# Optimization experiments

Measured on AMD Instinct MI355X. Metric: run time of the kernel, lower is better.

## Reference

```python
import jax, jax.numpy as jnp
import numpy as np

B, S, D, H = 4, 512, 1024, 16
HD = D // H
K_TOP = 8
MC_K = 8
EPS6 = 1e-6


def _affine(loc, scale, W, b):
    # Gaussian-diag affine: mu = x@W.T+b, var = scale^2 @ (W^2).T
    mu = loc @ W.T + b
    var = (scale ** 2) @ (W ** 2).T
    return mu, jnp.sqrt(var)


def _split(x):  # [B,S,D] -> [B,H,S,HD]
    return x.reshape(B, S, H, HD).transpose(0, 2, 1, 3)


def _combine(x):  # [B,H,S,HD] -> [B,S,D]
    return x.transpose(0, 2, 1, 3).reshape(B, S, D)


def _softmax_logit_normal(mu, var, excl_mask):
    # logit-normal softmax moment approximation (probit / delta method),
    # excluding masked positions (prob -> 0 there).
    adj = mu / jnp.sqrt(1.0 + (jnp.pi / 8.0) * var)
    adj = jnp.where(excl_mask, -1e9, adj)
    p = jax.nn.softmax(adj, axis=-1)
    v = (p * (1.0 - p)) ** 2 * var
    return p, v


def _forward(Q_loc, Q_scale, K_loc, K_scale, V_loc, V_scale,
             Wq, bq, Wk, bk, Wv, bv, Wo, bo, tau, eps):
    q_mu, q_sc = _affine(Q_loc, Q_scale, Wq, bq)
    k_mu, k_sc = _affine(K_loc, K_scale, Wk, bk)
    v_mu, v_sc = _affine(V_loc, V_scale, Wv, bv)

    # split heads; GaussianDiag round-trip adds 1e-6 to scale before squaring
    qm, qv = _split(q_mu), (_split(q_sc) + EPS6) ** 2
    km, kv = _split(k_mu), (_split(k_sc) + EPS6) ** 2
    vm, vv = _split(v_mu), (_split(v_sc) + EPS6) ** 2

    # bilinear moment: E[QK^T], Var[QK^T]
    S_mu = jnp.einsum('bhqd,bhkd->bhqk', qm, km)
    S_var = (jnp.einsum('bhqd,bhkd->bhqk', qm ** 2, kv)
             + jnp.einsum('bhqd,bhkd->bhqk', qv, km ** 2)
             + jnp.einsum('bhqd,bhkd->bhqk', qv, kv)) + EPS6

    s_mu = S_mu / jnp.sqrt(jnp.float32(HD))
    s_var = S_var / HD + EPS6

    l_mu = s_mu / tau
    l_var = s_var / (tau ** 2) + EPS6

    # top-k indices by mean logit
    topk_idx = jax.lax.top_k(l_mu, K_TOP)[1]  # [B,H,S,K_TOP]
    rows = jnp.arange(B * H * S)[:, None]
    mask = jnp.zeros((B * H * S, S), bool).at[rows, topk_idx.reshape(-1, K_TOP)].set(True)
    mask = mask.reshape(B, H, S, S)

    # MC-sample softmax (mc_k=8)
    std = jnp.sqrt(jnp.maximum(l_var, 1e-9))
    p_mean = jax.nn.softmax(l_mu[None] + std[None] * eps, axis=-1).mean(axis=0)

    # rest (non-top-k) logit-normal softmax moments
    rest_mean, rest_var = _softmax_logit_normal(l_mu, l_var, mask)

    top_out = jnp.where(mask, p_mean, rest_mean)
    top_out = top_out / jnp.maximum(top_out.sum(axis=-1, keepdims=True), 1e-12)

    # combine_top_rest: means add (variances do not feed the output path)
    attn_mu = top_out + rest_mean

    # linear combination with V distribution
    Y_mu = jnp.einsum('bhqk,bhkd->bhqd', attn_mu, vm)
    Y_var = jnp.einsum('bhqk,bhkd->bhqd', attn_mu ** 2, vv)
    Y_scale = jnp.sqrt(Y_var + EPS6)

    y_loc = _combine(Y_mu)
    y_scale = _combine(Y_scale) + EPS6

    out_loc = y_loc @ Wo.T + bo
    out_scale = jnp.sqrt((y_scale ** 2) @ (Wo ** 2).T)
    return out_loc, out_scale


def setup_inputs() -> dict:
    key = jax.random.key(0)
    ks = jax.random.split(key, 17)
    f32 = jnp.float32
    inp = {
        'Q_loc': jax.random.normal(ks[0], (B, S, D), f32),
        'Q_scale': jax.random.uniform(ks[1], (B, S, D), f32),
        'K_loc': jax.random.normal(ks[2], (B, S, D), f32),
        'K_scale': jax.random.uniform(ks[3], (B, S, D), f32),
        'V_loc': jax.random.normal(ks[4], (B, S, D), f32),
        'V_scale': jax.random.uniform(ks[5], (B, S, D), f32),
        'Wq': jax.random.normal(ks[6], (D, D), f32) * 0.02,
        'bq': jnp.zeros((D,), f32),
        'Wk': jax.random.normal(ks[7], (D, D), f32) * 0.02,
        'bk': jnp.zeros((D,), f32),
        'Wv': jax.random.normal(ks[8], (D, D), f32) * 0.02,
        'bv': jnp.zeros((D,), f32),
        'Wo': jax.random.normal(ks[9], (D, D), f32) * 0.02,
        'bo': jnp.zeros((D,), f32),
        'tau': jnp.array(1.0, f32),
        'eps': jax.random.normal(ks[10], (MC_K, B, H, S, S), f32),
    }
    return inp


def reference(Q_loc, Q_scale, K_loc, K_scale, V_loc, V_scale,
              Wq, bq, Wk, bk, Wv, bv, Wo, bo, tau, eps):
    return _forward(Q_loc, Q_scale, K_loc, K_scale, V_loc, V_scale,
                    Wq, bq, Wk, bk, Wv, bv, Wo, bo, tau, eps)
```

## Files before the change

kernel.cpp:

```cpp
#include <hip/hip_runtime.h>
#include <math.h>

#define B_ 4
#define S_ 512
#define D_ 1024
#define H_ 16
#define MCK 8
#define MS 2048
#define BHSS_ ((size_t)16777216)
#define BHS_  ((size_t)32768)

typedef __attribute__((ext_vector_type(8))) __bf16 bf16x8;
typedef __attribute__((ext_vector_type(4))) __bf16 bf16x4;
typedef __attribute__((ext_vector_type(4))) float f32x4;

__device__ __forceinline__ f32x4 mfma16(bf16x8 a, bf16x8 b, f32x4 c) {
  return __builtin_amdgcn_mfma_f32_16x16x32_bf16(a, b, c, 0, 0, 0);
}
__device__ __forceinline__ bf16x8 sq8(bf16x8 x) {
  bf16x8 r;
#pragma unroll
  for (int i = 0; i < 8; ++i) { float f = (float)x[i]; r[i] = (__bf16)(f * f); }
  return r;
}
__device__ __forceinline__ bf16x8 sq8s(bf16x8 h, bf16x8 l) {
  bf16x8 r;
#pragma unroll
  for (int i = 0; i < 8; ++i) { float f = (float)h[i] + (float)l[i]; r[i] = (__bf16)(f * f); }
  return r;
}
__device__ __forceinline__ float wave_max(float v) {
#pragma unroll
  for (int o = 32; o; o >>= 1) v = fmaxf(v, __shfl_xor(v, o));
  return v;
}
__device__ __forceinline__ float wave_sum(float v) {
#pragma unroll
  for (int o = 32; o; o >>= 1) v += __shfl_xor(v, o);
  return v;
}

__device__ __forceinline__ void unswz(int u, int& row, int& slot) {
  int row0 = ((u >> 2) ^ (u >> 4)) & 1;
  row = ((u >> 3) << 1) | row0;
  int s0 = (u ^ (u >> 2) ^ (u >> 4)) & 1;
  int s1 = ((u >> 1) ^ (u >> 3)) & 1;
  slot = (s1 << 1) | s0;
}
__device__ __forceinline__ int swz_el(int row, int slot) {
  return ((row * 4 + slot) ^ (row & 7)) * 8;
}
__device__ __forceinline__ void glds16(const void* gsrc, void* ldst) {
  __builtin_amdgcn_global_load_lds(
      (const __attribute__((address_space(1))) void*)gsrc,
      (__attribute__((address_space(3))) void*)ldst, 16, 0, 0);
}

__global__ __launch_bounds__(256) void conv_all(
    const float* __restrict__ l0, const float* __restrict__ s0,
    const float* __restrict__ l1, const float* __restrict__ s1,
    const float* __restrict__ l2, const float* __restrict__ s2,
    __bf16* h0, __bf16* o0, __bf16* v0,
    __bf16* h1, __bf16* o1, __bf16* v1,
    __bf16* h2, __bf16* o2, __bf16* v2,
    const float* __restrict__ w0, const float* __restrict__ w1,
    const float* __restrict__ w2, const float* __restrict__ w3,
    __bf16* wh0, __bf16* wo0, __bf16* wh1, __bf16* wo1,
    __bf16* wh2, __bf16* wo2, __bf16* wh3, __bf16* wo3)
{
  const int bid = blockIdx.x;
  if (bid < 3072) {
    const int tn = bid >> 10;
    const size_t i0 = ((size_t)(bid & 1023) * 256 + threadIdx.x) * 8;
    const float* L = tn == 0 ? l0 : tn == 1 ? l1 : l2;
    const float* S = tn == 0 ? s0 : tn == 1 ? s1 : s2;
    __bf16* Hh = tn == 0 ? h0 : tn == 1 ? h1 : h2;
    __bf16* Lo = tn == 0 ? o0 : tn == 1 ? o1 : o2;
    __bf16* V2 = tn == 0 ? v0 : tn == 1 ? v1 : v2;
    float4 x0 = *(const float4*)(L + i0), x1 = *(const float4*)(L + i0 + 4);
    float4 y0 = *(const float4*)(S + i0), y1 = *(const float4*)(S + i0 + 4);
    float xs[8] = {x0.x, x0.y, x0.z, x0.w, x1.x, x1.y, x1.z, x1.w};
    float ys[8] = {y0.x, y0.y, y0.z, y0.w, y1.x, y1.y, y1.z, y1.w};
    bf16x8 hh, ll, vv;
#pragma unroll
    for (int i = 0; i < 8; ++i) {
      __bf16 h = (__bf16)xs[i];
      hh[i] = h;
      ll[i] = (__bf16)(xs[i] - (float)h);
      vv[i] = (__bf16)(ys[i] * ys[i]);
    }
    *(bf16x8*)(Hh + i0) = hh;
    *(bf16x8*)(Lo + i0) = ll;
    *(bf16x8*)(V2 + i0) = vv;
  } else {
    const int b2 = bid - 3072;
    const int tn = b2 >> 9;
    const size_t i0 = ((size_t)(b2 & 511) * 256 + threadIdx.x) * 8;
    const float* W = tn == 0 ? w0 : tn == 1 ? w1 : tn == 2 ? w2 : w3;
    __bf16* Hh = tn == 0 ? wh0 : tn == 1 ? wh1 : tn == 2 ? wh2 : wh3;
    __bf16* Lo = tn == 0 ? wo0 : tn == 1 ? wo1 : tn == 2 ? wo2 : wo3;
    float4 x0 = *(const float4*)(W + i0), x1 = *(const float4*)(W + i0 + 4);
    float xs[8] = {x0.x, x0.y, x0.z, x0.w, x1.x, x1.y, x1.z, x1.w};
    bf16x8 hh, ll;
#pragma unroll
    for (int i = 0; i < 8; ++i) {
      __bf16 h = (__bf16)xs[i];
      hh[i] = h;
      ll[i] = (__bf16)(xs[i] - (float)h);
    }
    *(bf16x8*)(Hh + i0) = hh;
    *(bf16x8*)(Lo + i0) = ll;
  }
}

struct PArg {
  const __bf16 *Ah, *Al, *A2, *Wh, *Wl;
  const float* bias;
  __bf16 *P0, *P1, *P2, *P3;
  int epi;
};
struct PArg3 { PArg a[3]; };

#define LDSBUF 14336

__global__ __launch_bounds__(256, 2) void dgemm_qkv(PArg3 P3v)
{
  __shared__ __bf16 lds[2 * LDSBUF];
  const int lin = blockIdx.x + 8 * blockIdx.y + 256 * blockIdx.z;
  const int xcd = lin & 7;
  const int rest = lin >> 3;
  const int mi   = rest & 3;
  const int nblk = (rest >> 2) & 7;
  const int proj = rest >> 5;
  const PArg p = P3v.a[proj];
  const int m0 = (xcd + 8 * mi) * 64;
  const int n0 = nblk * 128;
  const int t = threadIdx.x, lane = t & 63, wid = t >> 6;
  int rA, sA; unswz(t, rA, sA);
  const size_t gA = (size_t)(m0 + rA) * D_ + sA * 8;
  const size_t gW0 = (size_t)(n0 + rA) * D_ + sA * 8;
  int rW1, sW1; unswz(t + 256, rW1, sW1);
  const size_t gW1 = (size_t)(n0 + rW1) * D_ + sW1 * 8;
  const int wofs = wid * 512;
  f32x4 accM[4][2] = {}; f32x4 accV[4][2] = {};
  const int fr = lane & 15, ks = lane >> 4;

  auto STAGE = [&](int buf, int k0) {
    __bf16* L = lds + buf * LDSBUF;
    glds16(p.Ah + gA + k0,  L + 0     + wofs);
    glds16(p.Al + gA + k0,  L + 2048  + wofs);
    glds16(p.A2 + gA + k0,  L + 4096  + wofs);
    glds16(p.Wh + gW0 + k0, L + 6144  + wofs);
    glds16(p.Wl + gW0 + k0, L + 10240 + wofs);
    glds16(p.Wh + gW1 + k0, L + 6144 + 2048 + wofs);
    glds16(p.Wl + gW1 + k0, L + 10240 + 2048 + wofs);
  };

  STAGE(0, 0);
  for (int tt = 0; tt < 32; ++tt) {
    const int cur = tt & 1;
    if (tt < 31) {
      STAGE(cur ^ 1, (tt + 1) * 32);
      asm volatile("s_waitcnt vmcnt(7)" ::: "memory");
    } else {
      asm volatile("s_waitcnt vmcnt(0)" ::: "memory");
    }
    __builtin_amdgcn_s_barrier();
    __builtin_amdgcn_sched_barrier(0);
    const __bf16* L = lds + cur * LDSBUF;
    bf16x8 fah[4], fal[4], fa2[4];
#pragma unroll
    for (int i = 0; i < 4; ++i) {
      int so = swz_el(i * 16 + fr, ks);
      fah[i] = *(const bf16x8*)(L + 0 + so);
      fal[i] = *(const bf16x8*)(L + 2048 + so);
      fa2[i] = *(const bf16x8*)(L + 4096 + so);
    }
#pragma unroll
    for (int j = 0; j < 2; ++j) {
      int so = swz_el(wid * 32 + j * 16 + fr, ks);
      bf16x8 fwh = *(const bf16x8*)(L + 6144 + so);
      bf16x8 fwl = *(const bf16x8*)(L + 10240 + so);
      bf16x8 fw2 = sq8s(fwh, fwl);
#pragma unroll
      for (int i = 0; i < 4; ++i) {
        accM[i][j] = mfma16(fah[i], fwh, accM[i][j]);
        accM[i][j] = mfma16(fah[i], fwl, accM[i][j]);
        accM[i][j] = mfma16(fal[i], fwh, accM[i][j]);
        accV[i][j] = mfma16(fa2[i], fw2, accV[i][j]);
      }
    }
    __builtin_amdgcn_s_barrier();
  }
  const int fq = lane >> 4;
#pragma unroll
  for (int j = 0; j < 2; ++j) {
    const int col = n0 + wid * 32 + j * 16 + fr;
    const float bcol = p.bias[col];
#pragma unroll
    for (int i = 0; i < 4; ++i) {
      const int row0 = m0 + i * 16 + fq * 4;
      f32x4 m_ = accM[i][j], v_ = accV[i][j];
      if (p.epi == 0) {
#pragma unroll
        for (int r = 0; r < 4; ++r) {
          size_t off = (size_t)(row0 + r) * D_ + col;
          float mu = m_[r] + bcol;
          __bf16 h = (__bf16)mu;
          float s = sqrtf(v_[r]) + 1e-6f;
          p.P0[off] = h;
          p.P1[off] = (__bf16)(mu - (float)h);
          p.P2[off] = (__bf16)(mu * mu);
          p.P3[off] = (__bf16)(s * s);
        }
      } else {
        const int b = row0 >> 9, ss0 = row0 & 511;
        const int hh = col >> 6, dd = col & 63;
        size_t base = ((size_t)(b * H_ + hh) * 64 + dd) * S_ + ss0;
        bf16x4 vh, vl, vq;
#pragma unroll
        for (int r = 0; r < 4; ++r) {
          float mu = m_[r] + bcol;
          __bf16 h = (__bf16)mu;
          vh[r] = h;
          vl[r] = (__bf16)(mu - (float)h);
          float s = sqrtf(v_[r]) + 1e-6f;
          vq[r] = (__bf16)(s * s);
        }
        *(bf16x4*)(p.P0 + base) = vh;
        *(bf16x4*)(p.P1 + base) = vl;
        *(bf16x4*)(p.P2 + base) = vq;
      }
    }
  }
}

__global__ __launch_bounds__(256, 2) void dgemm_o(
    const __bf16* __restrict__ Ah, const __bf16* __restrict__ Al, const __bf16* __restrict__ A2,
    const __bf16* __restrict__ Wh, const __bf16* __restrict__ Wl,
    const float* __restrict__ bias, float* __restrict__ O0, float* __restrict__ O1)
{
  __shared__ __bf16 lds[2 * LDSBUF];
  const int lin = blockIdx.x + 8 * blockIdx.y;
  const int xcd = lin & 7;
  const int rest = lin >> 3;
  const int mi   = rest & 3;
  const int nblk = rest >> 2;
  const int m0 = (xcd + 8 * mi) * 64;
  const int n0 = nblk * 128;
  const int t = threadIdx.x, lane = t & 63, wid = t >> 6;
  int rA, sA; unswz(t, rA, sA);
  const size_t gA = (size_t)(m0 + rA) * D_ + sA * 8;
  const size_t gW0 = (size_t)(n0 + rA) * D_ + sA * 8;
  int rW1, sW1; unswz(t + 256, rW1, sW1);
  const size_t gW1 = (size_t)(n0 + rW1) * D_ + sW1 * 8;
  const int wofs = wid * 512;
  f32x4 accM[4][2] = {}; f32x4 accV[4][2] = {};
  const int fr = lane & 15, ks = lane >> 4;

  auto STAGE = [&](int buf, int k0) {
    __bf16* L = lds + buf * LDSBUF;
    glds16(Ah + gA + k0,  L + 0     + wofs);
    glds16(Al + gA + k0,  L + 2048  + wofs);
    glds16(A2 + gA + k0,  L + 4096  + wofs);
    glds16(Wh + gW0 + k0, L + 6144  + wofs);
    glds16(Wl + gW0 + k0, L + 10240 + wofs);
    glds16(Wh + gW1 + k0, L + 6144 + 2048 + wofs);
    glds16(Wl + gW1 + k0, L + 10240 + 2048 + wofs);
  };

  STAGE(0, 0);
  for (int tt = 0; tt < 32; ++tt) {
    const int cur = tt & 1;
    if (tt < 31) {
      STAGE(cur ^ 1, (tt + 1) * 32);
      asm volatile("s_waitcnt vmcnt(7)" ::: "memory");
    } else {
      asm volatile("s_waitcnt vmcnt(0)" ::: "memory");
    }
    __builtin_amdgcn_s_barrier();
    __builtin_amdgcn_sched_barrier(0);
    const __bf16* L = lds + cur * LDSBUF;
    bf16x8 fah[4], fal[4], fa2[4];
#pragma unroll
    for (int i = 0; i < 4; ++i) {
      int so = swz_el(i * 16 + fr, ks);
      fah[i] = *(const bf16x8*)(L + 0 + so);
      fal[i] = *(const bf16x8*)(L + 2048 + so);
      fa2[i] = *(const bf16x8*)(L + 4096 + so);
    }
#pragma unroll
    for (int j = 0; j < 2; ++j) {
      int so = swz_el(wid * 32 + j * 16 + fr, ks);
      bf16x8 fwh = *(const bf16x8*)(L + 6144 + so);
      bf16x8 fwl = *(const bf16x8*)(L + 10240 + so);
      bf16x8 fw2 = sq8s(fwh, fwl);
#pragma unroll
      for (int i = 0; i < 4; ++i) {
        accM[i][j] = mfma16(fah[i], fwh, accM[i][j]);
        accM[i][j] = mfma16(fah[i], fwl, accM[i][j]);
        accM[i][j] = mfma16(fal[i], fwh, accM[i][j]);
        accV[i][j] = mfma16(fa2[i], fw2, accV[i][j]);
      }
    }
    __builtin_amdgcn_s_barrier();
  }
  const int fq = lane >> 4;
#pragma unroll
  for (int j = 0; j < 2; ++j) {
    const int col = n0 + wid * 32 + j * 16 + fr;
    const float bcol = bias[col];
#pragma unroll
    for (int i = 0; i < 4; ++i) {
      const int row0 = m0 + i * 16 + fq * 4;
      f32x4 m_ = accM[i][j], v_ = accV[i][j];
#pragma unroll
      for (int r = 0; r < 4; ++r) {
        size_t off = (size_t)(row0 + r) * D_ + col;
        O0[off] = m_[r] + bcol;
        O1[off] = sqrtf(v_[r]);
      }
    }
  }
}

__global__ __launch_bounds__(256) void score_mfma(
    const __bf16* __restrict__ qh, const __bf16* __restrict__ ql,
    const __bf16* __restrict__ q2, const __bf16* __restrict__ qv,
    const __bf16* __restrict__ kh, const __bf16* __restrict__ kl,
    const __bf16* __restrict__ k2, const __bf16* __restrict__ kv,
    float* __restrict__ lmu, __bf16* __restrict__ lvar,
    const float* __restrict__ taup)
{
  __shared__ __bf16 sQ[4][64][32];
  __shared__ __bf16 sK[4][64][32];
  const int t = threadIdx.x;
  const int lane = t & 63, wid = t >> 6;
  const int wm = wid >> 1, wn = wid & 1;
  const int lin = blockIdx.x + 8 * blockIdx.y + 64 * blockIdx.z;
  const int xcd = lin & 7;
  const int rest = lin >> 3;
  const int tile = rest & 63;
  const int bh = xcd + 8 * (rest >> 6);
  const int kk0 = (tile & 7) * 64, q0 = (tile >> 3) * 64;
  const int b = bh >> 4, h = bh & 15;
  const size_t hb = ((size_t)b * S_) * D_ + (size_t)h * 64;
  f32x4 accM[2][2] = {}; f32x4 accV[2][2] = {};
  const int crow = t >> 2, ccol = (t & 3) * 8;
  for (int d0 = 0; d0 < 64; d0 += 32) {
    size_t gq = hb + (size_t)(q0 + crow) * D_ + d0 + ccol;
    size_t gk = hb + (size_t)(kk0 + crow) * D_ + d0 + ccol;
    bf16x8 a0 = *(const bf16x8*)(qh + gq);
    bf16x8 a1 = *(const bf16x8*)(ql + gq);
    bf16x8 a2 = *(const bf16x8*)(q2 + gq);
    bf16x8 a3 = *(const bf16x8*)(qv + gq);
    bf16x8 b0 = *(const bf16x8*)(kh + gk);
    bf16x8 b1 = *(const bf16x8*)(kl + gk);
    bf16x8 b2 = *(const bf16x8*)(k2 + gk);
    bf16x8 b3 = *(const bf16x8*)(kv + gk);
    __syncthreads();
    *(bf16x8*)&sQ[0][crow][ccol] = a0;
    *(bf16x8*)&sQ[1][crow][ccol] = a1;
    *(bf16x8*)&sQ[2][crow][ccol] = a2;
    *(bf16x8*)&sQ[3][crow][ccol] = a3;
    *(bf16x8*)&sK[0][crow][ccol] = b0;
    *(bf16x8*)&sK[1][crow][ccol] = b1;
    *(bf16x8*)&sK[2][crow][ccol] = b2;
    *(bf16x8*)&sK[3][crow][ccol] = b3;
    __syncthreads();
    const int fr = lane & 15, kc = (lane >> 4) * 8;
    bf16x8 fqh[2], fql[2], fq2[2], fqv[2];
#pragma unroll
    for (int i = 0; i < 2; ++i) {
      int r = wm * 32 + i * 16 + fr;
      fqh[i] = *(const bf16x8*)&sQ[0][r][kc];
      fql[i] = *(const bf16x8*)&sQ[1][r][kc];
      fq2[i] = *(const bf16x8*)&sQ[2][r][kc];
      fqv[i] = *(const bf16x8*)&sQ[3][r][kc];
    }
#pragma unroll
    for (int j = 0; j < 2; ++j) {
      int r = wn * 32 + j * 16 + fr;
      bf16x8 fkh = *(const bf16x8*)&sK[0][r][kc];
      bf16x8 fkl = *(const bf16x8*)&sK[1][r][kc];
      bf16x8 fk2 = *(const bf16x8*)&sK[2][r][kc];
      bf16x8 fkv = *(const bf16x8*)&sK[3][r][kc];
#pragma unroll
      for (int i = 0; i < 2; ++i) {
        accM[i][j] = mfma16(fqh[i], fkh, accM[i][j]);
        accM[i][j] = mfma16(fqh[i], fkl, accM[i][j]);
        accM[i][j] = mfma16(fql[i], fkh, accM[i][j]);
        accV[i][j] = mfma16(fq2[i], fkv, accV[i][j]);
        accV[i][j] = mfma16(fqv[i], fk2, accV[i][j]);
        accV[i][j] = mfma16(fqv[i], fkv, accV[i][j]);
      }
    }
  }
  const float itau = 1.0f / *taup;
  const int fr = lane & 15, fq = lane >> 4;
#pragma unroll
  for (int i = 0; i < 2; ++i)
#pragma unroll
    for (int j = 0; j < 2; ++j) {
      const int col = kk0 + wn * 32 + j * 16 + fr;
      const int row0 = q0 + wm * 32 + i * 16 + fq * 4;
      f32x4 m_ = accM[i][j], v_ = accV[i][j];
#pragma unroll
      for (int r = 0; r < 4; ++r) {
        size_t off = ((size_t)bh * S_ + row0 + r) * S_ + col;
        lmu[off] = m_[r] * 0.125f * itau;
        float lv = ((v_[r] + 1e-6f) * (1.0f / 64.0f) + 1e-6f) * itau * itau + 1e-6f;
        lvar[off] = (__bf16)lv;
      }
    }
}

__global__ __launch_bounds__(256) void attn_kernel(
    const float* __restrict__ lmu, const __bf16* __restrict__ lvar,
    const float* __restrict__ eps, __bf16* __restrict__ ah, __bf16* __restrict__ al)
{
  const int wid = threadIdx.x >> 6;
  const int lane = threadIdx.x & 63;
  const size_t r = (size_t)blockIdx.x * 4 + wid;
  const float* mrow = lmu + r * S_;
  const __bf16* vrow = lvar + r * S_;
  const int c0 = lane * 4;
  float mu[8], va[8], sd[8];
  {
    float4 m0 = *(const float4*)(mrow + c0);
    float4 m1 = *(const float4*)(mrow + 256 + c0);
    mu[0] = m0.x; mu[1] = m0.y; mu[2] = m0.z; mu[3] = m0.w;
    mu[4] = m1.x; mu[5] = m1.y; mu[6] = m1.z; mu[7] = m1.w;
    bf16x4 v0 = *(const bf16x4*)(vrow + c0);
    bf16x4 v1 = *(const bf16x4*)(vrow + 256 + c0);
#pragma unroll
    for (int i = 0; i < 4; ++i) { va[i] = (float)v0[i]; va[4 + i] = (float)v1[i]; }
  }
#pragma unroll
  for (int i = 0; i < 8; ++i) sd[i] = sqrtf(fmaxf(va[i], 1e-9f));
  unsigned sel = 0;
  float x[8];
#pragma unroll
  for (int i = 0; i < 8; ++i) x[i] = mu[i];
  for (int tsel = 0; tsel < 8; ++tsel) {
    float bv = -INFINITY; int bi = 0x7fffffff;
#pragma unroll
    for (int i = 0; i < 8; ++i) {
      int gi = (i < 4) ? (c0 + i) : (256 + c0 + i - 4);
      if (x[i] > bv || (x[i] == bv && gi < bi)) { bv = x[i]; bi = gi; }
    }
    for (int o = 32; o; o >>= 1) {
      float ov = __shfl_xor(bv, o); int oi = __shfl_xor(bi, o);
      if (ov > bv || (ov == bv && oi < bi)) { bv = ov; bi = oi; }
    }
    int half = bi >> 8;
    int rem = bi & 255;
    if ((rem >> 2) == lane) {
      int slot = (rem & 3) + 4 * half;
      sel |= 1u << slot;
      x[slot] = -INFINITY;
    }
  }
  float pacc[8] = {0, 0, 0, 0, 0, 0, 0, 0};
  for (int mc = 0; mc < MCK; ++mc) {
    const float* ep = eps + (size_t)mc * BHSS_ + r * S_;
    float4 e0 = *(const float4*)(ep + c0);
    float4 e1 = *(const float4*)(ep + 256 + c0);
    float xv[8];
    xv[0] = mu[0] + sd[0] * e0.x; xv[1] = mu[1] + sd[1] * e0.y;
    xv[2] = mu[2] + sd[2] * e0.z; xv[3] = mu[3] + sd[3] * e0.w;
    xv[4] = mu[4] + sd[4] * e1.x; xv[5] = mu[5] + sd[5] * e1.y;
    xv[6] = mu[6] + sd[6] * e1.z; xv[7] = mu[7] + sd[7] * e1.w;
    float m = -INFINITY;
#pragma unroll
    for (int i = 0; i < 8; ++i) m = fmaxf(m, xv[i]);
    m = wave_max(m);
    float e[8], zs = 0.f;
#pragma unroll
    for (int i = 0; i < 8; ++i) { e[i] = __expf(xv[i] - m); zs += e[i]; }
    zs = wave_sum(zs);
    float inv = 1.0f / zs;
#pragma unroll
    for (int i = 0; i < 8; ++i) pacc[i] += e[i] * inv;
  }
  float adj[8];
#pragma unroll
  for (int i = 0; i < 8; ++i) {
    float a = mu[i] / sqrtf(1.0f + 0.39269908169872414f * va[i]);
    adj[i] = ((sel >> i) & 1u) ? -1e9f : a;
  }
  float m2 = -INFINITY;
#pragma unroll
  for (int i = 0; i < 8; ++i) m2 = fmaxf(m2, adj[i]);
  m2 = wave_max(m2);
  float e2[8], z2 = 0.f;
#pragma unroll
  for (int i = 0; i < 8; ++i) { e2[i] = __expf(adj[i] - m2); z2 += e2[i]; }
  z2 = wave_sum(z2);
  float inv2 = 1.0f / z2;
  float rest[8], tout[8], s = 0.f;
#pragma unroll
  for (int i = 0; i < 8; ++i) {
    rest[i] = e2[i] * inv2;
    tout[i] = ((sel >> i) & 1u) ? pacc[i] * 0.125f : rest[i];
    s += tout[i];
  }
  s = wave_sum(s);
  float rn = 1.0f / fmaxf(s, 1e-12f);
  bf16x4 oh0, oh1, ol0, ol1;
#pragma unroll
  for (int i = 0; i < 4; ++i) {
    float o = tout[i] * rn + rest[i];
    __bf16 h = (__bf16)o;
    oh0[i] = h; ol0[i] = (__bf16)(o - (float)h);
    float o1 = tout[4 + i] * rn + rest[4 + i];
    __bf16 h1 = (__bf16)o1;
    oh1[i] = h1; ol1[i] = (__bf16)(o1 - (float)h1);
  }
  *(bf16x4*)(ah + r * S_ + c0) = oh0;
  *(bf16x4*)(ah + r * S_ + 256 + c0) = oh1;
  *(bf16x4*)(al + r * S_ + c0) = ol0;
  *(bf16x4*)(al + r * S_ + 256 + c0) = ol1;
}

__global__ __launch_bounds__(256) void pv_mfma(
    const __bf16* __restrict__ ah_, const __bf16* __restrict__ al_,
    const __bf16* __restrict__ vTh, const __bf16* __restrict__ vTl,
    const __bf16* __restrict__ vTv,
    __bf16* __restrict__ yh, __bf16* __restrict__ yl, __bf16* __restrict__ ys2)
{
  __shared__ __bf16 sA[2][64][32];
  __shared__ __bf16 sV[3][64][32];
  const int t = threadIdx.x;
  const int lane = t & 63, wid = t >> 6;
  const int wm = wid >> 1, wn = wid & 1;
  const int lin = blockIdx.x + 8 * blockIdx.y;
  const int xcd = lin & 7;
  const int rest = lin >> 3;
  const int q0 = (rest & 7) * 64;
  const int bh = xcd + 8 * (rest >> 3);
  const int b = bh >> 4, h = bh & 15;
  const __bf16* Ah = ah_ + (size_t)bh * S_ * S_;
  const __bf16* Al = al_ + (size_t)bh * S_ * S_;
  const __bf16* Vh = vTh + (size_t)bh * 64 * S_;
  const __bf16* Vl = vTl + (size_t)bh * 64 * S_;
  const __bf16* Vv = vTv + (size_t)bh * 64 * S_;
  f32x4 accM[2][2] = {}; f32x4 accV[2][2] = {};
  const int crow = t >> 2, ccol = (t & 3) * 8;
  for (int k0 = 0; k0 < S_; k0 += 32) {
    size_t gA = (size_t)(q0 + crow) * S_ + k0 + ccol;
    size_t gV = (size_t)crow * S_ + k0 + ccol;
    bf16x8 a0 = *(const bf16x8*)(Ah + gA);
    bf16x8 a1 = *(const bf16x8*)(Al + gA);
    bf16x8 v0 = *(const bf16x8*)(Vh + gV);
    bf16x8 v1 = *(const bf16x8*)(Vl + gV);
    bf16x8 v2 = *(const bf16x8*)(Vv + gV);
    __syncthreads();
    *(bf16x8*)&sA[0][crow][ccol] = a0;
    *(bf16x8*)&sA[1][crow][ccol] = a1;
    *(bf16x8*)&sV[0][crow][ccol] = v0;
    *(bf16x8*)&sV[1][crow][ccol] = v1;
    *(bf16x8*)&sV[2][crow][ccol] = v2;
    __syncthreads();
    const int fr = lane & 15, kc = (lane >> 4) * 8;
    bf16x8 fah[2], fal[2], fa2[2];
#pragma unroll
    for (int i = 0; i < 2; ++i) {
      int rr = wm * 32 + i * 16 + fr;
      fah[i] = *(const bf16x8*)&sA[0][rr][kc];
      fal[i] = *(const bf16x8*)&sA[1][rr][kc];
      fa2[i] = sq8(fah[i]);
    }
#pragma unroll
    for (int j = 0; j < 2; ++j) {
      int rr = wn * 32 + j * 16 + fr;
      bf16x8 fvh = *(const bf16x8*)&sV[0][rr][kc];
      bf16x8 fvl = *(const bf16x8*)&sV[1][rr][kc];
      bf16x8 fvv = *(const bf16x8*)&sV[2][rr][kc];
#pragma unroll
      for (int i = 0; i < 2; ++i) {
        accM[i][j] = mfma16(fah[i], fvh, accM[i][j]);
        accM[i][j] = mfma16(fah[i], fvl, accM[i][j]);
        accM[i][j] = mfma16(fal[i], fvh, accM[i][j]);
        accV[i][j] = mfma16(fa2[i], fvv, accV[i][j]);
      }
    }
  }
  const int fr = lane & 15, fq = lane >> 4;
#pragma unroll
  for (int i = 0; i < 2; ++i)
#pragma unroll
    for (int j = 0; j < 2; ++j) {
      const int col = h * 64 + wn * 32 + j * 16 + fr;
      const int row0 = b * S_ + q0 + wm * 32 + i * 16 + fq * 4;
      f32x4 m_ = accM[i][j], v_ = accV[i][j];
#pragma unroll
      for (int r = 0; r < 4; ++r) {
        size_t off = (size_t)(row0 + r) * D_ + col;
        float mu = m_[r];
        __bf16 hh = (__bf16)mu;
        float ss = sqrtf(v_[r] + 1e-6f) + 1e-6f;
        yh[off] = hh;
        yl[off] = (__bf16)(mu - (float)hh);
        ys2[off] = (__bf16)(ss * ss);
      }
    }
}

extern "C" void kernel_launch(void* const* d_in, const int* in_sizes, int n_in,
                              void* d_out, int out_size, void* d_ws, size_t ws_size,
                              hipStream_t stream)
{
  const float* Qloc = (const float*)d_in[0];
  const float* Qsc  = (const float*)d_in[1];
  const float* Kloc = (const float*)d_in[2];
  const float* Ksc  = (const float*)d_in[3];
  const float* Vloc = (const float*)d_in[4];
  const float* Vsc  = (const float*)d_in[5];
  const float* Wq = (const float*)d_in[6];  const float* bq = (const float*)d_in[7];
  const float* Wk = (const float*)d_in[8];  const float* bk = (const float*)d_in[9];
  const float* Wv = (const float*)d_in[10]; const float* bv = (const float*)d_in[11];
  const float* Wo = (const float*)d_in[12]; const float* bo = (const float*)d_in[13];
  const float* tau = (const float*)d_in[14];
  const float* eps = (const float*)d_in[15];

  const size_t P = (size_t)MS * D_;
  const size_t DD = (size_t)D_ * D_;
  char* w = (char*)d_ws;
  auto carve = [&](size_t bytes) -> char* {
    char* p = w; w += (bytes + 255) & ~(size_t)255; return p;
  };
  __bf16* cQh = (__bf16*)carve(P * 2); __bf16* cQl = (__bf16*)carve(P * 2); __bf16* cQ2 = (__bf16*)carve(P * 2);
  __bf16* cKh = (__bf16*)carve(P * 2); __bf16* cKl = (__bf16*)carve(P * 2); __bf16* cK2 = (__bf16*)carve(P * 2);
  __bf16* cVh = (__bf16*)carve(P * 2); __bf16* cVl = (__bf16*)carve(P * 2); __bf16* cV2 = (__bf16*)carve(P * 2);
  __bf16* wqh = (__bf16*)carve(DD * 2); __bf16* wql = (__bf16*)carve(DD * 2);
  __bf16* wkh = (__bf16*)carve(DD * 2); __bf16* wkl = (__bf16*)carve(DD * 2);
  __bf16* wvh = (__bf16*)carve(DD * 2); __bf16* wvl = (__bf16*)carve(DD * 2);
  __bf16* woh = (__bf16*)carve(DD * 2); __bf16* wol = (__bf16*)carve(DD * 2);
  __bf16* qmh = (__bf16*)carve(P * 2); __bf16* qml = (__bf16*)carve(P * 2);
  __bf16* qm2 = (__bf16*)carve(P * 2); __bf16* qmv = (__bf16*)carve(P * 2);
  __bf16* kmh = (__bf16*)carve(P * 2); __bf16* kml = (__bf16*)carve(P * 2);
  __bf16* km2 = (__bf16*)carve(P * 2); __bf16* kmv = (__bf16*)carve(P * 2);
  __bf16* vTh = (__bf16*)carve(P * 2); __bf16* vTl = (__bf16*)carve(P * 2); __bf16* vTv = (__bf16*)carve(P * 2);
  float*  lmu = (float*)carve(BHSS_ * 4);
  __bf16* lvr = (__bf16*)carve(BHSS_ * 2);
  __bf16* ath = (__bf16*)carve(BHSS_ * 2);
  __bf16* atl = (__bf16*)carve(BHSS_ * 2);
  __bf16* yh = (__bf16*)carve(P * 2); __bf16* yl = (__bf16*)carve(P * 2); __bf16* ys2 = (__bf16*)carve(P * 2);
  float* out_loc = (float*)d_out;
  float* out_sc  = out_loc + P;

  dim3 blk(256);
  conv_all<<<5120, blk, 0, stream>>>(Qloc, Qsc, Kloc, Ksc, Vloc, Vsc,
                                     cQh, cQl, cQ2, cKh, cKl, cK2, cVh, cVl, cV2,
                                     Wq, Wk, Wv, Wo,
                                     wqh, wql, wkh, wkl, wvh, wvl, woh, wol);
  PArg3 pq;
  pq.a[0] = PArg{cQh, cQl, cQ2, wqh, wql, bq, qmh, qml, qm2, qmv, 0};
  pq.a[1] = PArg{cKh, cKl, cK2, wkh, wkl, bk, kmh, kml, km2, kmv, 0};
  pq.a[2] = PArg{cVh, cVl, cV2, wvh, wvl, bv, vTh, vTl, vTv, nullptr, 1};
  dgemm_qkv<<<dim3(8, 32, 3), blk, 0, stream>>>(pq);
  score_mfma<<<dim3(8, 8, 64), blk, 0, stream>>>(qmh, qml, qm2, qmv, kmh, kml, km2, kmv, lmu, lvr, tau);
  attn_kernel<<<dim3((unsigned)(BHS_ / 4)), blk, 0, stream>>>(lmu, lvr, eps, ath, atl);
  pv_mfma<<<dim3(8, 64), blk, 0, stream>>>(ath, atl, vTh, vTl, vTv, yh, yl, ys2);
  dgemm_o<<<dim3(8, 32), blk, 0, stream>>>(yh, yl, ys2, woh, wol, bo, out_loc, out_sc);
}
```

Baseline: 348.1 us.

## Fuse score, stochastic softmax and PV into one LDS-resident attention kernel

Replaces the three kernels score_mfma, attn_kernel and pv_mfma with a single fused_attn kernel. Each 512-thread block owns a 32-query tile of one head. It computes the mean and variance logits into LDS, runs top-k, the MC-sample softmax and the logit-normal softmax on them in place, stores the split bf16 attention weights back in LDS, then multiplies by V. This removes the global write and read of the full logit-mean, logit-variance and attention-weight tensors. In exchange, about 148 KB of LDS per block allows only one block per CU, which lowers occupancy while the large eps tensor is streamed. K and V are also re-read by every query tile.

```diff
diff --git a/kernel.cpp b/kernel.cpp
--- a/kernel.cpp
+++ b/kernel.cpp
@@ -324,287 +324,305 @@
   }
 }
 
-__global__ __launch_bounds__(256) void score_mfma(
+__global__ __launch_bounds__(512, 1) void fused_attn(
     const __bf16* __restrict__ qh, const __bf16* __restrict__ ql,
     const __bf16* __restrict__ q2, const __bf16* __restrict__ qv,
     const __bf16* __restrict__ kh, const __bf16* __restrict__ kl,
     const __bf16* __restrict__ k2, const __bf16* __restrict__ kv,
-    float* __restrict__ lmu, __bf16* __restrict__ lvar,
-    const float* __restrict__ taup)
+    const __bf16* __restrict__ vTh, const __bf16* __restrict__ vTl,
+    const __bf16* __restrict__ vTv,
+    const float* __restrict__ eps, const float* __restrict__ taup,
+    __bf16* __restrict__ yh, __bf16* __restrict__ yl, __bf16* __restrict__ ys2)
 {
-  __shared__ __bf16 sQ[4][64][32];
-  __shared__ __bf16 sK[4][64][32];
-  const int t = threadIdx.x;
-  const int lane = t & 63, wid = t >> 6;
-  const int wm = wid >> 1, wn = wid & 1;
-  const int lin = blockIdx.x + 8 * blockIdx.y + 64 * blockIdx.z;
-  const int xcd = lin & 7;
-  const int rest = lin >> 3;
-  const int tile = rest & 63;
-  const int bh = xcd + 8 * (rest >> 6);
-  const int kk0 = (tile & 7) * 64, q0 = (tile >> 3) * 64;
+  __shared__ __align__(16) char smem[151296];
+  float*  LMU  = (float*)smem;
+  __bf16* ATTH = (__bf16*)smem;
+  __bf16* ATTL = (__bf16*)(smem + 33024);
+  __bf16* LVAR = (__bf16*)(smem + 66048);
+  __bf16* QST  = (__bf16*)(smem + 99072);
+  __bf16* KST  = (__bf16*)(smem + 116480);
+  __bf16* VST  = (__bf16*)(smem + 99072);
+
+  const int t = threadIdx.x, lane = t & 63, wid = t >> 6;
+  const int lin = blockIdx.x;
+  const int xcd = lin & 7, rest = lin >> 3;
+  const int qb = rest & 15, bh = xcd + 8 * (rest >> 4);
+  const int q0 = qb * 32;
   const int b = bh >> 4, h = bh & 15;
-  const size_t hb = ((size_t)b * S_) * D_ + (size_t)h * 64;
-  f32x4 accM[2][2] = {}; f32x4 accV[2][2] = {};
-  const int crow = t >> 2, ccol = (t & 3) * 8;
-  for (int d0 = 0; d0 < 64; d0 += 32) {
-    size_t gq = hb + (size_t)(q0 + crow) * D_ + d0 + ccol;
-    size_t gk = hb + (size_t)(kk0 + crow) * D_ + d0 + ccol;
-    bf16x8 a0 = *(const bf16x8*)(qh + gq);
-    bf16x8 a1 = *(const bf16x8*)(ql + gq);
-    bf16x8 a2 = *(const bf16x8*)(q2 + gq);
-    bf16x8 a3 = *(const bf16x8*)(qv + gq);
-    bf16x8 b0 = *(const bf16x8*)(kh + gk);
-    bf16x8 b1 = *(const bf16x8*)(kl + gk);
-    bf16x8 b2 = *(const bf16x8*)(k2 + gk);
-    bf16x8 b3 = *(const bf16x8*)(kv + gk);
-    __syncthreads();
-    *(bf16x8*)&sQ[0][crow][ccol] = a0;
-    *(bf16x8*)&sQ[1][crow][ccol] = a1;
-    *(bf16x8*)&sQ[2][crow][ccol] = a2;
-    *(bf16x8*)&sQ[3][crow][ccol] = a3;
-    *(bf16x8*)&sK[0][crow][ccol] = b0;
-    *(bf16x8*)&sK[1][crow][ccol] = b1;
-    *(bf16x8*)&sK[2][crow][ccol] = b2;
-    *(bf16x8*)&sK[3][crow][ccol] = b3;
-    __syncthreads();
-    const int fr = lane & 15, kc = (lane >> 4) * 8;
-    bf16x8 fqh[2], fql[2], fq2[2], fqv[2];
-#pragma unroll
-    for (int i = 0; i < 2; ++i) {
-      int r = wm * 32 + i * 16 + fr;
-      fqh[i] = *(const bf16x8*)&sQ[0][r][kc];
-      fql[i] = *(const bf16x8*)&sQ[1][r][kc];
-      fq2[i] = *(const bf16x8*)&sQ[2][r][kc];
-      fqv[i] = *(const bf16x8*)&sQ[3][r][kc];
-    }
-#pragma unroll
-    for (int j = 0; j < 2; ++j) {
-      int r = wn * 32 + j * 16 + fr;
-      bf16x8 fkh = *(const bf16x8*)&sK[0][r][kc];
-      bf16x8 fkl = *(const bf16x8*)&sK[1][r][kc];
-      bf16x8 fk2 = *(const bf16x8*)&sK[2][r][kc];
-      bf16x8 fkv = *(const bf16x8*)&sK[3][r][kc];
-#pragma unroll
-      for (int i = 0; i < 2; ++i) {
-        accM[i][j] = mfma16(fqh[i], fkh, accM[i][j]);
-        accM[i][j] = mfma16(fqh[i], fkl, accM[i][j]);
-        accM[i][j] = mfma16(fql[i], fkh, accM[i][j]);
-        accV[i][j] = mfma16(fq2[i], fkv, accV[i][j]);
-        accV[i][j] = mfma16(fqv[i], fk2, accV[i][j]);
-        accV[i][j] = mfma16(fqv[i], fkv, accV[i][j]);
-      }
-    }
-  }
+  const size_t qgbase = ((size_t)b * S_ + q0) * D_ + h * 64;
+  const size_t kgbase = ((size_t)b * S_) * D_ + h * 64;
   const float itau = 1.0f / *taup;
   const int fr = lane & 15, fq = lane >> 4;
-#pragma unroll
-  for (int i = 0; i < 2; ++i)
-#pragma unroll
-    for (int j = 0; j < 2; ++j) {
-      const int col = kk0 + wn * 32 + j * 16 + fr;
-      const int row0 = q0 + wm * 32 + i * 16 + fq * 4;
-      f32x4 m_ = accM[i][j], v_ = accV[i][j];
-#pragma unroll
-      for (int r = 0; r < 4; ++r) {
-        size_t off = ((size_t)bh * S_ + row0 + r) * S_ + col;
-        lmu[off] = m_[r] * 0.125f * itau;
-        float lv = ((v_[r] + 1e-6f) * (1.0f / 64.0f) + 1e-6f) * itau * itau + 1e-6f;
-        lvar[off] = (__bf16)lv;
-      }
-    }
-}
-
-__global__ __launch_bounds__(256) void attn_kernel(
-    const float* __restrict__ lmu, const __bf16* __restrict__ lvar,
-    const float* __restrict__ eps, __bf16* __restrict__ ah, __bf16* __restrict__ al)
-{
-  const int wid = threadIdx.x >> 6;
-  const int lane = threadIdx.x & 63;
-  const size_t r = (size_t)blockIdx.x * 4 + wid;
-  const float* mrow = lmu + r * S_;
-  const __bf16* vrow = lvar + r * S_;
+
+  {
+    const int row = t >> 4, c4 = (t & 15) * 4;
+    const size_t g = qgbase + (size_t)row * D_ + c4;
+    const int l = row * 68 + c4;
+    *(bf16x4*)(QST + 0 * 2176 + l) = *(const bf16x4*)(qh + g);
+    *(bf16x4*)(QST + 1 * 2176 + l) = *(const bf16x4*)(ql + g);
+    *(bf16x4*)(QST + 2 * 2176 + l) = *(const bf16x4*)(q2 + g);
+    *(bf16x4*)(QST + 3 * 2176 + l) = *(const bf16x4*)(qv + g);
+  }
+
+  const int path = wid >> 2;
+  const int p = wid & 3;
+  for (int ck = 0; ck < 8; ++ck) {
+    if (ck) __syncthreads();
+    {
+      const int row = t >> 3, c8 = (t & 7) * 8;
+      const size_t g = kgbase + (size_t)(ck * 64 + row) * D_ + c8;
+      const int l = row * 68 + c8;
+      *(bf16x8*)(KST + 0 * 4352 + l) = *(const bf16x8*)(kh + g);
+      *(bf16x8*)(KST + 1 * 4352 + l) = *(const bf16x8*)(kl + g);
+      *(bf16x8*)(KST + 2 * 4352 + l) = *(const bf16x8*)(k2 + g);
+      *(bf16x8*)(KST + 3 * 4352 + l) = *(const bf16x8*)(kv + g);
+    }
+    __syncthreads();
+    f32x4 acc[2] = {};
+    if (path == 0) {
+#pragma unroll
+      for (int ds = 0; ds < 2; ++ds) {
+        bf16x8 fqh_[2], fql_[2];
+#pragma unroll
+        for (int i = 0; i < 2; ++i) {
+          int qoff = (i * 16 + fr) * 68 + ds * 32 + fq * 8;
+          fqh_[i] = *(const bf16x8*)(QST + 0 * 2176 + qoff);
+          fql_[i] = *(const bf16x8*)(QST + 1 * 2176 + qoff);
+        }
+        int koff = (p * 16 + fr) * 68 + ds * 32 + fq * 8;
+        bf16x8 fkh_ = *(const bf16x8*)(KST + 0 * 4352 + koff);
+        bf16x8 fkl_ = *(const bf16x8*)(KST + 1 * 4352 + koff);
+#pragma unroll
+        for (int i = 0; i < 2; ++i) {
+          acc[i] = mfma16(fqh_[i], fkh_, acc[i]);
+          acc[i] = mfma16(fqh_[i], fkl_, acc[i]);
+          acc[i] = mfma16(fql_[i], fkh_, acc[i]);
+        }
+      }
+      const int col = ck * 64 + p * 16 + fr;
+#pragma unroll
+      for (int i = 0; i < 2; ++i) {
+        const int row0 = i * 16 + fq * 4;
+#pragma unroll
+        for (int r = 0; r < 4; ++r)
+          LMU[(row0 + r) * 516 + col] = acc[i][r] * 0.125f * itau;
+      }
+    } else {
+#pragma unroll
+      for (int ds = 0; ds < 2; ++ds) {
+        bf16x8 fq2_[2], fqv_[2];
+#pragma unroll
+        for (int i = 0; i < 2; ++i) {
+          int qoff = (i * 16 + fr) * 68 + ds * 32 + fq * 8;
+          fq2_[i] = *(const bf16x8*)(QST + 2 * 2176 + qoff);
+          fqv_[i] = *(const bf16x8*)(QST + 3 * 2176 + qoff);
+        }
+        int koff = (p * 16 + fr) * 68 + ds * 32 + fq * 8;
+        bf16x8 fk2_ = *(const bf16x8*)(KST + 2 * 4352 + koff);
+        bf16x8 fkv_ = *(const bf16x8*)(KST + 3 * 4352 + koff);
+#pragma unroll
+        for (int i = 0; i < 2; ++i) {
+          acc[i] = mfma16(fq2_[i], fkv_, acc[i]);
+          acc[i] = mfma16(fqv_[i], fk2_, acc[i]);
+          acc[i] = mfma16(fqv_[i], fkv_, acc[i]);
+        }
+      }
+      const int col = ck * 64 + p * 16 + fr;
+#pragma unroll
+      for (int i = 0; i < 2; ++i) {
+        const int row0 = i * 16 + fq * 4;
+#pragma unroll
+        for (int r = 0; r < 4; ++r) {
+          float lv = ((acc[i][r] + 1e-6f) * (1.0f / 64.0f) + 1e-6f) * itau * itau + 1e-6f;
+          LVAR[(row0 + r) * 516 + col] = (__bf16)lv;
+        }
+      }
+    }
+  }
+  __syncthreads();
+
   const int c0 = lane * 4;
-  float mu[8], va[8], sd[8];
+  float o_keep[4][8];
+#pragma unroll
+  for (int rr = 0; rr < 4; ++rr) {
+    const int R = wid * 4 + rr;
+    float mu[8], va[8], sd[8];
+    {
+      float4 m0 = *(const float4*)(LMU + R * 516 + c0);
+      float4 m1 = *(const float4*)(LMU + R * 516 + 256 + c0);
+      mu[0] = m0.x; mu[1] = m0.y; mu[2] = m0.z; mu[3] = m0.w;
+      mu[4] = m1.x; mu[5] = m1.y; mu[6] = m1.z; mu[7] = m1.w;
+      bf16x4 v0 = *(const bf16x4*)(LVAR + R * 516 + c0);
+      bf16x4 v1 = *(const bf16x4*)(LVAR + R * 516 + 256 + c0);
+#pragma unroll
+      for (int i = 0; i < 4; ++i) { va[i] = (float)v0[i]; va[4 + i] = (float)v1[i]; }
+    }
+#pragma unroll
+    for (int i = 0; i < 8; ++i) sd[i] = sqrtf(fmaxf(va[i], 1e-9f));
+    unsigned sel = 0;
+    float x[8];
+#pragma unroll
+    for (int i = 0; i < 8; ++i) x[i] = mu[i];
+    for (int tsel = 0; tsel < 8; ++tsel) {
+      float bv = -INFINITY; int bi = 0x7fffffff;
+#pragma unroll
+      for (int i = 0; i < 8; ++i) {
+        int gi = (i < 4) ? (c0 + i) : (256 + c0 + i - 4);
+        if (x[i] > bv || (x[i] == bv && gi < bi)) { bv = x[i]; bi = gi; }
+      }
+      for (int o = 32; o; o >>= 1) {
+        float ov = __shfl_xor(bv, o); int oi = __shfl_xor(bi, o);
+        if (ov > bv || (ov == bv && oi < bi)) { bv = ov; bi = oi; }
+      }
+      int half = bi >> 8;
+      int rem = bi & 255;
+      if ((rem >> 2) == lane) {
+        int slot = (rem & 3) + 4 * half;
+        sel |= 1u << slot;
+        x[slot] = -INFINITY;
+      }
+    }
+    float pacc[8] = {0, 0, 0, 0, 0, 0, 0, 0};
+    const size_t rg = ((size_t)bh * S_ + q0 + R) * S_;
+    for (int mc = 0; mc < MCK; ++mc) {
+      const float* ep = eps + (size_t)mc * BHSS_ + rg;
+      float4 e0 = *(const float4*)(ep + c0);
+      float4 e1 = *(const float4*)(ep + 256 + c0);
+      float xv[8];
+      xv[0] = mu[0] + sd[0] * e0.x; xv[1] = mu[1] + sd[1] * e0.y;
+      xv[2] = mu[2] + sd[2] * e0.z; xv[3] = mu[3] + sd[3] * e0.w;
+      xv[4] = mu[4] + sd[4] * e1.x; xv[5] = mu[5] + sd[5] * e1.y;
+      xv[6] = mu[6] + sd[6] * e1.z; xv[7] = mu[7] + sd[7] * e1.w;
+      float m = -INFINITY;
+#pragma unroll
+      for (int i = 0; i < 8; ++i) m = fmaxf(m, xv[i]);
+      m = wave_max(m);
+      float e[8], zs = 0.f;
+#pragma unroll
+      for (int i = 0; i < 8; ++i) { e[i] = __expf(xv[i] - m); zs += e[i]; }
+      zs = wave_sum(zs);
+      float inv = 1.0f / zs;
+#pragma unroll
+      for (int i = 0; i < 8; ++i) pacc[i] += e[i] * inv;
+    }
+    float adj[8];
+#pragma unroll
+    for (int i = 0; i < 8; ++i) {
+      float a = mu[i] / sqrtf(1.0f + 0.39269908169872414f * va[i]);
+      adj[i] = ((sel >> i) & 1u) ? -1e9f : a;
+    }
+    float m2 = -INFINITY;
+#pragma unroll
+    for (int i = 0; i < 8; ++i) m2 = fmaxf(m2, adj[i]);
+    m2 = wave_max(m2);
+    float e2[8], z2 = 0.f;
+#pragma unroll
+    for (int i = 0; i < 8; ++i) { e2[i] = __expf(adj[i] - m2); z2 += e2[i]; }
+    z2 = wave_sum(z2);
+    float inv2 = 1.0f / z2;
+    float rst[8], tout[8], s = 0.f;
+#pragma unroll
+    for (int i = 0; i < 8; ++i) {
+      rst[i] = e2[i] * inv2;
+      tout[i] = ((sel >> i) & 1u) ? pacc[i] * 0.125f : rst[i];
+      s += tout[i];
+    }
+    s = wave_sum(s);
+    float rn = 1.0f / fmaxf(s, 1e-12f);
+#pragma unroll
+    for (int i = 0; i < 8; ++i) o_keep[rr][i] = tout[i] * rn + rst[i];
+  }
+  __syncthreads();
+#pragma unroll
+  for (int rr = 0; rr < 4; ++rr) {
+    const int R = wid * 4 + rr;
+    bf16x4 oh0, oh1, ol0, ol1;
+#pragma unroll
+    for (int i = 0; i < 4; ++i) {
+      float o = o_keep[rr][i];
+      __bf16 hh = (__bf16)o;
+      oh0[i] = hh; ol0[i] = (__bf16)(o - (float)hh);
+      float o1 = o_keep[rr][4 + i];
+      __bf16 h1 = (__bf16)o1;
+      oh1[i] = h1; ol1[i] = (__bf16)(o1 - (float)h1);
+    }
+    *(bf16x4*)(ATTH + R * 516 + c0) = oh0;
+    *(bf16x4*)(ATTH + R * 516 + 256 + c0) = oh1;
+    *(bf16x4*)(ATTL + R * 516 + c0) = ol0;
+    *(bf16x4*)(ATTL + R * 516 + 256 + c0) = ol1;
+  }
+  __syncthreads();
+
+  const int j = wid & 3;
+  f32x4 pvacc[2] = {};
+  for (int ck2 = 0; ck2 < 4; ++ck2) {
+    if (ck2) __syncthreads();
+    {
+#pragma unroll
+      for (int u = 0; u < 2; ++u) {
+        const int s = t + u * 512;
+        const int row = s >> 4, cg = (s & 15) * 8;
+        const size_t g = ((size_t)bh * 64 + row) * S_ + ck2 * 128 + cg;
+        const int l = row * 132 + cg;
+        *(bf16x8*)(VST + 0 * 8448 + l) = *(const bf16x8*)(vTh + g);
+        *(bf16x8*)(VST + 1 * 8448 + l) = *(const bf16x8*)(vTl + g);
+        *(bf16x8*)(VST + 2 * 8448 + l) = *(const bf16x8*)(vTv + g);
+      }
+    }
+    __syncthreads();
+#pragma unroll
+    for (int ksub = 0; ksub < 4; ++ksub) {
+      const int ka = ck2 * 128 + ksub * 32 + fq * 8;
+      bf16x8 ah_[2];
+#pragma unroll
+      for (int i = 0; i < 2; ++i)
+        ah_[i] = *(const bf16x8*)(ATTH + (i * 16 + fr) * 516 + ka);
+      const int voff = (j * 16 + fr) * 132 + ksub * 32 + fq * 8;
+      if (wid < 4) {
+        bf16x8 al_[2];
+#pragma unroll
+        for (int i = 0; i < 2; ++i)
+          al_[i] = *(const bf16x8*)(ATTL + (i * 16 + fr) * 516 + ka);
+        bf16x8 fvh = *(const bf16x8*)(VST + 0 * 8448 + voff);
+        bf16x8 fvl = *(const bf16x8*)(VST + 1 * 8448 + voff);
+#pragma unroll
+        for (int i = 0; i < 2; ++i) {
+          pvacc[i] = mfma16(ah_[i], fvh, pvacc[i]);
+          pvacc[i] = mfma16(ah_[i], fvl, pvacc[i]);
+          pvacc[i] = mfma16(al_[i], fvh, pvacc[i]);
+        }
+      } else {
+        bf16x8 fvv = *(const bf16x8*)(VST + 2 * 8448 + voff);
+#pragma unroll
+        for (int i = 0; i < 2; ++i)
+          pvacc[i] = mfma16(sq8(ah_[i]), fvv, pvacc[i]);
+      }
+    }
+  }
   {
-    float4 m0 = *(const float4*)(mrow + c0);
-    float4 m1 = *(const float4*)(mrow + 256 + c0);
-    mu[0] = m0.x; mu[1] = m0.y; mu[2] = m0.z; mu[3] = m0.w;
-    mu[4] = m1.x; mu[5] = m1.y; mu[6] = m1.z; mu[7] = m1.w;
-    bf16x4 v0 = *(const bf16x4*)(vrow + c0);
-    bf16x4 v1 = *(const bf16x4*)(vrow + 256 + c0);
-#pragma unroll
-    for (int i = 0; i < 4; ++i) { va[i] = (float)v0[i]; va[4 + i] = (float)v1[i]; }
-  }
-#pragma unroll
-  for (int i = 0; i < 8; ++i) sd[i] = sqrtf(fmaxf(va[i], 1e-9f));
-  unsigned sel = 0;
-  float x[8];
-#pragma unroll
-  for (int i = 0; i < 8; ++i) x[i] = mu[i];
-  for (int tsel = 0; tsel < 8; ++tsel) {
-    float bv = -INFINITY; int bi = 0x7fffffff;
-#pragma unroll
-    for (int i = 0; i < 8; ++i) {
-      int gi = (i < 4) ? (c0 + i) : (256 + c0 + i - 4);
-      if (x[i] > bv || (x[i] == bv && gi < bi)) { bv = x[i]; bi = gi; }
-    }
-    for (int o = 32; o; o >>= 1) {
-      float ov = __shfl_xor(bv, o); int oi = __shfl_xor(bi, o);
-      if (ov > bv || (ov == bv && oi < bi)) { bv = ov; bi = oi; }
-    }
-    int half = bi >> 8;
-    int rem = bi & 255;
-    if ((rem >> 2) == lane) {
-      int slot = (rem & 3) + 4 * half;
-      sel |= 1u << slot;
-      x[slot] = -INFINITY;
-    }
-  }
-  float pacc[8] = {0, 0, 0, 0, 0, 0, 0, 0};
-  for (int mc = 0; mc < MCK; ++mc) {
-    const float* ep = eps + (size_t)mc * BHSS_ + r * S_;
-    float4 e0 = *(const float4*)(ep + c0);
-    float4 e1 = *(const float4*)(ep + 256 + c0);
-    float xv[8];
-    xv[0] = mu[0] + sd[0] * e0.x; xv[1] = mu[1] + sd[1] * e0.y;
-    xv[2] = mu[2] + sd[2] * e0.z; xv[3] = mu[3] + sd[3] * e0.w;
-    xv[4] = mu[4] + sd[4] * e1.x; xv[5] = mu[5] + sd[5] * e1.y;
-    xv[6] = mu[6] + sd[6] * e1.z; xv[7] = mu[7] + sd[7] * e1.w;
-    float m = -INFINITY;
-#pragma unroll
-    for (int i = 0; i < 8; ++i) m = fmaxf(m, xv[i]);
-    m = wave_max(m);
-    float e[8], zs = 0.f;
-#pragma unroll
-    for (int i = 0; i < 8; ++i) { e[i] = __expf(xv[i] - m); zs += e[i]; }
-    zs = wave_sum(zs);
-    float inv = 1.0f / zs;
-#pragma unroll
-    for (int i = 0; i < 8; ++i) pacc[i] += e[i] * inv;
-  }
-  float adj[8];
-#pragma unroll
-  for (int i = 0; i < 8; ++i) {
-    float a = mu[i] / sqrtf(1.0f + 0.39269908169872414f * va[i]);
-    adj[i] = ((sel >> i) & 1u) ? -1e9f : a;
-  }
-  float m2 = -INFINITY;
-#pragma unroll
-  for (int i = 0; i < 8; ++i) m2 = fmaxf(m2, adj[i]);
-  m2 = wave_max(m2);
-  float e2[8], z2 = 0.f;
-#pragma unroll
-  for (int i = 0; i < 8; ++i) { e2[i] = __expf(adj[i] - m2); z2 += e2[i]; }
-  z2 = wave_sum(z2);
-  float inv2 = 1.0f / z2;
-  float rest[8], tout[8], s = 0.f;
-#pragma unroll
-  for (int i = 0; i < 8; ++i) {
-    rest[i] = e2[i] * inv2;
-    tout[i] = ((sel >> i) & 1u) ? pacc[i] * 0.125f : rest[i];
-    s += tout[i];
-  }
-  s = wave_sum(s);
-  float rn = 1.0f / fmaxf(s, 1e-12f);
-  bf16x4 oh0, oh1, ol0, ol1;
-#pragma unroll
-  for (int i = 0; i < 4; ++i) {
-    float o = tout[i] * rn + rest[i];
-    __bf16 h = (__bf16)o;
-    oh0[i] = h; ol0[i] = (__bf16)(o - (float)h);
-    float o1 = tout[4 + i] * rn + rest[4 + i];
-    __bf16 h1 = (__bf16)o1;
-    oh1[i] = h1; ol1[i] = (__bf16)(o1 - (float)h1);
-  }
-  *(bf16x4*)(ah + r * S_ + c0) = oh0;
-  *(bf16x4*)(ah + r * S_ + 256 + c0) = oh1;
-  *(bf16x4*)(al + r * S_ + c0) = ol0;
-  *(bf16x4*)(al + r * S_ + 256 + c0) = ol1;
-}
-
-__global__ __launch_bounds__(256) void pv_mfma(
-    const __bf16* __restrict__ ah_, const __bf16* __restrict__ al_,
-    const __bf16* __restrict__ vTh, const __bf16* __restrict__ vTl,
-    const __bf16* __restrict__ vTv,
-    __bf16* __restrict__ yh, __bf16* __restrict__ yl, __bf16* __restrict__ ys2)
-{
-  __shared__ __bf16 sA[2][64][32];
-  __shared__ __bf16 sV[3][64][32];
-  const int t = threadIdx.x;
-  const int lane = t & 63, wid = t >> 6;
-  const int wm = wid >> 1, wn = wid & 1;
-  const int lin = blockIdx.x + 8 * blockIdx.y;
-  const int xcd = lin & 7;
-  const int rest = lin >> 3;
-  const int q0 = (rest & 7) * 64;
-  const int bh = xcd + 8 * (rest >> 3);
-  const int b = bh >> 4, h = bh & 15;
-  const __bf16* Ah = ah_ + (size_t)bh * S_ * S_;
-  const __bf16* Al = al_ + (size_t)bh * S_ * S_;
-  const __bf16* Vh = vTh + (size_t)bh * 64 * S_;
-  const __bf16* Vl = vTl + (size_t)bh * 64 * S_;
-  const __bf16* Vv = vTv + (size_t)bh * 64 * S_;
-  f32x4 accM[2][2] = {}; f32x4 accV[2][2] = {};
-  const int crow = t >> 2, ccol = (t & 3) * 8;
-  for (int k0 = 0; k0 < S_; k0 += 32) {
-    size_t gA = (size_t)(q0 + crow) * S_ + k0 + ccol;
-    size_t gV = (size_t)crow * S_ + k0 + ccol;
-    bf16x8 a0 = *(const bf16x8*)(Ah + gA);
-    bf16x8 a1 = *(const bf16x8*)(Al + gA);
-    bf16x8 v0 = *(const bf16x8*)(Vh + gV);
-    bf16x8 v1 = *(const bf16x8*)(Vl + gV);
-    bf16x8 v2 = *(const bf16x8*)(Vv + gV);
-    __syncthreads();
-    *(bf16x8*)&sA[0][crow][ccol] = a0;
-    *(bf16x8*)&sA[1][crow][ccol] = a1;
-    *(bf16x8*)&sV[0][crow][ccol] = v0;
-    *(bf16x8*)&sV[1][crow][ccol] = v1;
-    *(bf16x8*)&sV[2][crow][ccol] = v2;
-    __syncthreads();
-    const int fr = lane & 15, kc = (lane >> 4) * 8;
-    bf16x8 fah[2], fal[2], fa2[2];
+    const int col = h * 64 + j * 16 + fr;
 #pragma unroll
     for (int i = 0; i < 2; ++i) {
-      int rr = wm * 32 + i * 16 + fr;
-      fah[i] = *(const bf16x8*)&sA[0][rr][kc];
-      fal[i] = *(const bf16x8*)&sA[1][rr][kc];
-      fa2[i] = sq8(fah[i]);
-    }
-#pragma unroll
-    for (int j = 0; j < 2; ++j) {
-      int rr = wn * 32 + j * 16 + fr;
-      bf16x8 fvh = *(const bf16x8*)&sV[0][rr][kc];
-      bf16x8 fvl = *(const bf16x8*)&sV[1][rr][kc];
-      bf16x8 fvv = *(const bf16x8*)&sV[2][rr][kc];
-#pragma unroll
-      for (int i = 0; i < 2; ++i) {
-        accM[i][j] = mfma16(fah[i], fvh, accM[i][j]);
-        accM[i][j] = mfma16(fah[i], fvl, accM[i][j]);
-        accM[i][j] = mfma16(fal[i], fvh, accM[i][j]);
-        accV[i][j] = mfma16(fa2[i], fvv, accV[i][j]);
-      }
-    }
-  }
-  const int fr = lane & 15, fq = lane >> 4;
-#pragma unroll
-  for (int i = 0; i < 2; ++i)
-#pragma unroll
-    for (int j = 0; j < 2; ++j) {
-      const int col = h * 64 + wn * 32 + j * 16 + fr;
-      const int row0 = b * S_ + q0 + wm * 32 + i * 16 + fq * 4;
-      f32x4 m_ = accM[i][j], v_ = accV[i][j];
-#pragma unroll
-      for (int r = 0; r < 4; ++r) {
-        size_t off = (size_t)(row0 + r) * D_ + col;
-        float mu = m_[r];
-        __bf16 hh = (__bf16)mu;
-        float ss = sqrtf(v_[r] + 1e-6f) + 1e-6f;
-        yh[off] = hh;
-        yl[off] = (__bf16)(mu - (float)hh);
-        ys2[off] = (__bf16)(ss * ss);
-      }
-    }
+      const int grow0 = b * S_ + q0 + i * 16 + fq * 4;
+      if (wid < 4) {
+#pragma unroll
+        for (int r = 0; r < 4; ++r) {
+          size_t off = (size_t)(grow0 + r) * D_ + col;
+          float m = pvacc[i][r];
+          __bf16 hh = (__bf16)m;
+          yh[off] = hh;
+          yl[off] = (__bf16)(m - (float)hh);
+        }
+      } else {
+#pragma unroll
+        for (int r = 0; r < 4; ++r) {
+          size_t off = (size_t)(grow0 + r) * D_ + col;
+          float ss = sqrtf(pvacc[i][r] + 1e-6f) + 1e-6f;
+          ys2[off] = (__bf16)(ss * ss);
+        }
+      }
+    }
+  }
 }
 
 extern "C" void kernel_launch(void* const* d_in, const int* in_sizes, int n_in,
@@ -642,10 +660,6 @@
   __bf16* kmh = (__bf16*)carve(P * 2); __bf16* kml = (__bf16*)carve(P * 2);
   __bf16* km2 = (__bf16*)carve(P * 2); __bf16* kmv = (__bf16*)carve(P * 2);
   __bf16* vTh = (__bf16*)carve(P * 2); __bf16* vTl = (__bf16*)carve(P * 2); __bf16* vTv = (__bf16*)carve(P * 2);
-  float*  lmu = (float*)carve(BHSS_ * 4);
-  __bf16* lvr = (__bf16*)carve(BHSS_ * 2);
-  __bf16* ath = (__bf16*)carve(BHSS_ * 2);
-  __bf16* atl = (__bf16*)carve(BHSS_ * 2);
   __bf16* yh = (__bf16*)carve(P * 2); __bf16* yl = (__bf16*)carve(P * 2); __bf16* ys2 = (__bf16*)carve(P * 2);
   float* out_loc = (float*)d_out;
   float* out_sc  = out_loc + P;
@@ -660,8 +674,7 @@
   pq.a[1] = PArg{cKh, cKl, cK2, wkh, wkl, bk, kmh, kml, km2, kmv, 0};
   pq.a[2] = PArg{cVh, cVl, cV2, wvh, wvl, bv, vTh, vTl, vTv, nullptr, 1};
   dgemm_qkv<<<dim3(8, 32, 3), blk, 0, stream>>>(pq);
-  score_mfma<<<dim3(8, 8, 64), blk, 0, stream>>>(qmh, qml, qm2, qmv, kmh, kml, km2, kmv, lmu, lvr, tau);
-  attn_kernel<<<dim3((unsigned)(BHS_ / 4)), blk, 0, stream>>>(lmu, lvr, eps, ath, atl);
-  pv_mfma<<<dim3(8, 64), blk, 0, stream>>>(ath, atl, vTh, vTl, vTv, yh, yl, ys2);
+  fused_attn<<<1024, 512, 0, stream>>>(qmh, qml, qm2, qmv, kmh, kml, km2, kmv,
+                                       vTh, vTl, vTv, eps, tau, yh, yl, ys2);
   dgemm_o<<<dim3(8, 32), blk, 0, stream>>>(yh, yl, ys2, woh, wol, bo, out_loc, out_sc);
 }
```

New measurement: 627.1 us. 80.2% more time.
